# Optimization experiments

Hardware: AMD Instinct MI355X
Metric: run time of the kernel (lower is better)

## Reference

```python
import jax, jax.numpy as jnp
import numpy as np


def setup_inputs() -> dict:
    key = jax.random.key(0)
    ks = jax.random.split(key, 10)
    b, l, d, n, dc = 4, 4096, 768, 16, 4
    w = lambda k, shape, s: jax.random.normal(k, shape, jnp.float32) * s
    return {
        "x": w(ks[0], (b, l, d), 1.0),
        "state": jnp.zeros((b, d, n), jnp.float32),
        "W_in": w(ks[1], (d, 2 * d), 0.02),      # in_proj (expand_factor=2)
        "conv_w": w(ks[2], (d, dc), 0.1),          # depthwise conv1d weight [d_model, d_conv]
        "conv_b": w(ks[3], (d,), 0.02),
        "W_x": w(ks[4], (d, 2 * n), 0.02),         # x_proj -> (B, C)
        "W_dt": w(ks[5], (d, d), 0.02),
        "b_dt": w(ks[6], (d,), 0.02),
        "A_log": w(ks[7], (d, n), 0.1),
        "D": jnp.ones((d,), jnp.float32),
        "W_out": w(ks[8], (d, d), 0.02),
    }


def reference(x, state, W_in, conv_w, conv_b, W_x, W_dt, b_dt, A_log, D, W_out):
    b, l, d = x.shape
    n = A_log.shape[1]
    dc = conv_w.shape[1]

    xz = x @ W_in                              # [b,l,2d]
    x_ssm, z = jnp.split(xz, 2, axis=-1)       # each [b,l,d]

    # causal depthwise conv1d (torch pads by dc-1 both sides then truncates to l)
    xp = jnp.pad(x_ssm, ((0, 0), (dc - 1, 0), (0, 0)))
    x_conv = conv_b
    for k in range(dc):
        x_conv = x_conv + xp[:, k:k + l, :] * conv_w[:, k]
    x_ssm = jax.nn.silu(x_conv)

    A = -jnp.exp(A_log)                        # [d,n]
    dt = jax.nn.softplus(x_ssm @ W_dt + b_dt)  # [b,l,d]
    B_seq, C_seq = jnp.split(x_ssm @ W_x, 2, axis=-1)  # each [b,l,n]

    # selective scan: state[b,d,n] = state*exp(dt*A) + B*x ; y = <state,C> + D*x
    def step(s, inp):
        x_t, B_t, C_t, dt_t = inp              # [b,d],[b,n],[b,n],[b,d]
        dA = jnp.exp(dt_t[:, :, None] * A)     # [b,d,n]
        s = s * dA + B_t[:, None, :] * x_t[:, :, None]
        y = jnp.einsum('bdn,bn->bd', s, C_t) + D * x_t
        return s, y

    s0 = jnp.zeros((b, d, n), x.dtype)         # parallel_selective_scan starts from zeros
    _, ys = jax.lax.scan(
        step, s0,
        (x_ssm.transpose(1, 0, 2), B_seq.transpose(1, 0, 2),
         C_seq.transpose(1, 0, 2), dt.transpose(1, 0, 2)))
    y = ys.transpose(1, 0, 2)                  # [b,l,d]

    y = y * jax.nn.silu(z)
    out = y @ W_out
    # use_fused_ops path returns the (unchanged) incoming state as new_state
    return out, state
```

## Files before the change

kernel.cpp:

```cpp
#include <hip/hip_runtime.h>
#include <hip/hip_bf16.h>
#include <cstdint>
#include <cstddef>

constexpr int Bc = 4, Lc = 4096, Dc = 768, Nc = 16;
constexpr int M_TOT = Bc * Lc;
constexpr int NCH = 128;
constexpr int TCH = Lc / NCH;
constexpr int Kd = 768;
constexpr int TWO_D = 1536;
constexpr int NDTBC = 896;

typedef __attribute__((ext_vector_type(8))) short short8v;
typedef __attribute__((ext_vector_type(4))) float f32x4;

__device__ __forceinline__ float fexp2(float x) {
#if __has_builtin(__builtin_amdgcn_exp2f)
    return __builtin_amdgcn_exp2f(x);
#else
    return exp2f(x);
#endif
}
__device__ __forceinline__ float softplusf(float x) {
    return (x > 20.0f) ? x : __logf(1.0f + __expf(x));
}
__device__ __forceinline__ float siluf(float x) {
    return x / (1.0f + __expf(-x));
}
__device__ __forceinline__ float bf16lo(uint32_t v) {
    return __uint_as_float(v << 16);
}
__device__ __forceinline__ float bf16hi(uint32_t v) {
    return __uint_as_float(v & 0xffff0000u);
}

__device__ __forceinline__ void swizzled_tile(int& row0, int& col0)
{
    const int nwg = gridDim.x * gridDim.y;
    const int bid = blockIdx.y * gridDim.x + blockIdx.x;
    const int swz = (bid & 7) * (nwg >> 3) + (bid >> 3);
    row0 = (swz / gridDim.x) * 128;
    col0 = (swz % gridDim.x) * 128;
}

__global__ __launch_bounds__(256)
void gemm_bf16_f32(const __hip_bfloat16* __restrict__ Ab,
                   const __hip_bfloat16* __restrict__ Wt,
                   int N, float* __restrict__ out0)
{
    __shared__ __hip_bfloat16 Asm[128 * 32];
    __shared__ __hip_bfloat16 Bsm[128 * 32];
    const int tid = threadIdx.x;
    const int w = tid >> 6, lane = tid & 63;
    const int lr = lane & 15, lc = lane >> 4;
    int row0, col0;
    swizzled_tile(row0, col0);
    const int wrow = (w >> 1) * 64, wcol = (w & 1) * 64;

    const int srow = lane >> 2;
    const int scol = (lane & 3) * 8;

    f32x4 acc[4][4] = {};

    const int KT = Kd / 32;
    for (int kt = 0; kt < KT; ++kt) {
        if (kt) __syncthreads();
        #pragma unroll
        for (int i = 0; i < 2; ++i) {
            const int seg = w * 2 + i;
            const __hip_bfloat16* asrc =
                Ab + (size_t)(row0 + seg * 16 + srow) * Kd + kt * 32 + scol;
            const __hip_bfloat16* bsrc =
                Wt + (size_t)(col0 + seg * 16 + srow) * Kd + kt * 32 + scol;
            __builtin_amdgcn_global_load_lds(
                (const __attribute__((address_space(1))) void*)asrc,
                (__attribute__((address_space(3))) void*)(Asm + seg * 512), 16, 0, 0);
            __builtin_amdgcn_global_load_lds(
                (const __attribute__((address_space(1))) void*)bsrc,
                (__attribute__((address_space(3))) void*)(Bsm + seg * 512), 16, 0, 0);
        }
        asm volatile("s_waitcnt vmcnt(0)" ::: "memory");
        __syncthreads();

        short8v a[4], b[4];
        #pragma unroll
        for (int m = 0; m < 4; ++m)
            a[m] = *(const short8v*)((char*)Asm + (wrow + m * 16 + lr) * 64 + lc * 16);
        #pragma unroll
        for (int nf = 0; nf < 4; ++nf)
            b[nf] = *(const short8v*)((char*)Bsm + (wcol + nf * 16 + lr) * 64 + lc * 16);
        #pragma unroll
        for (int m = 0; m < 4; ++m)
            #pragma unroll
            for (int nf = 0; nf < 4; ++nf)
                acc[m][nf] = __builtin_amdgcn_mfma_f32_16x16x32_bf16(
                    a[m], b[nf], acc[m][nf], 0, 0, 0);
    }

    #pragma unroll
    for (int m = 0; m < 4; ++m)
        #pragma unroll
        for (int nf = 0; nf < 4; ++nf)
            #pragma unroll
            for (int j = 0; j < 4; ++j) {
                const int rg = row0 + wrow + m * 16 + lc * 4 + j;
                const int cg = col0 + wcol + nf * 16 + lr;
                out0[(size_t)rg * N + cg] = acc[m][nf][j];
            }
}

__global__ __launch_bounds__(256)
void gemm_bf16_b16(const __hip_bfloat16* __restrict__ Ab,
                   const __hip_bfloat16* __restrict__ Wt,
                   int N, __hip_bfloat16* __restrict__ outb)
{
    __shared__ __hip_bfloat16 Asm[128 * 32];
    __shared__ __hip_bfloat16 Bsm[128 * 32];
    const int tid = threadIdx.x;
    const int w = tid >> 6, lane = tid & 63;
    const int lr = lane & 15, lc = lane >> 4;
    int row0, col0;
    swizzled_tile(row0, col0);
    const int wrow = (w >> 1) * 64, wcol = (w & 1) * 64;

    const int srow = lane >> 2;
    const int scol = (lane & 3) * 8;

    f32x4 acc[4][4] = {};

    const int KT = Kd / 32;
    for (int kt = 0; kt < KT; ++kt) {
        if (kt) __syncthreads();
        #pragma unroll
        for (int i = 0; i < 2; ++i) {
            const int seg = w * 2 + i;
            const __hip_bfloat16* asrc =
                Ab + (size_t)(row0 + seg * 16 + srow) * Kd + kt * 32 + scol;
            const __hip_bfloat16* bsrc =
                Wt + (size_t)(col0 + seg * 16 + srow) * Kd + kt * 32 + scol;
            __builtin_amdgcn_global_load_lds(
                (const __attribute__((address_space(1))) void*)asrc,
                (__attribute__((address_space(3))) void*)(Asm + seg * 512), 16, 0, 0);
            __builtin_amdgcn_global_load_lds(
                (const __attribute__((address_space(1))) void*)bsrc,
                (__attribute__((address_space(3))) void*)(Bsm + seg * 512), 16, 0, 0);
        }
        asm volatile("s_waitcnt vmcnt(0)" ::: "memory");
        __syncthreads();

        short8v a[4], b[4];
        #pragma unroll
        for (int m = 0; m < 4; ++m)
            a[m] = *(const short8v*)((char*)Asm + (wrow + m * 16 + lr) * 64 + lc * 16);
        #pragma unroll
        for (int nf = 0; nf < 4; ++nf)
            b[nf] = *(const short8v*)((char*)Bsm + (wcol + nf * 16 + lr) * 64 + lc * 16);
        #pragma unroll
        for (int m = 0; m < 4; ++m)
            #pragma unroll
            for (int nf = 0; nf < 4; ++nf)
                acc[m][nf] = __builtin_amdgcn_mfma_f32_16x16x32_bf16(
                    a[m], b[nf], acc[m][nf], 0, 0, 0);
    }

    #pragma unroll
    for (int m = 0; m < 4; ++m)
        #pragma unroll
        for (int nf = 0; nf < 4; ++nf)
            #pragma unroll
            for (int j = 0; j < 4; ++j) {
                const int rg = row0 + wrow + m * 16 + lc * 4 + j;
                const int cg = col0 + wcol + nf * 16 + lr;
                outb[(size_t)rg * N + cg] = __float2bfloat16(acc[m][nf][j]);
            }
}

__global__ __launch_bounds__(256)
void to_bf16_kernel(const float* __restrict__ src, __hip_bfloat16* __restrict__ dst, int n4)
{
    const int i = blockIdx.x * 256 + threadIdx.x;
    if (i >= n4) return;
    const float4 v = ((const float4*)src)[i];
    dst[i * 4 + 0] = __float2bfloat16(v.x);
    dst[i * 4 + 1] = __float2bfloat16(v.y);
    dst[i * 4 + 2] = __float2bfloat16(v.z);
    dst[i * 4 + 3] = __float2bfloat16(v.w);
}

__global__ __launch_bounds__(256)
void wtrans_tile(const float* __restrict__ src, __hip_bfloat16* __restrict__ dst, int N)
{
    __shared__ float tile[32][33];
    const int n0 = blockIdx.x * 32, k0 = blockIdx.y * 32;
    const int tx = threadIdx.x & 31, ty = threadIdx.x >> 5;
    #pragma unroll
    for (int r = 0; r < 4; ++r) {
        const int k = ty + r * 8;
        tile[k][tx] = src[(size_t)(k0 + k) * N + n0 + tx];
    }
    __syncthreads();
    #pragma unroll
    for (int r = 0; r < 4; ++r) {
        const int n = ty + r * 8;
        dst[(size_t)(n0 + n) * Kd + k0 + tx] = __float2bfloat16(tile[tx][n]);
    }
}

__global__ __launch_bounds__(256)
void aprep_kernel(const float* __restrict__ A_log, float* __restrict__ Abuf)
{
    const int i = blockIdx.x * 256 + threadIdx.x;
    if (i < Dc * Nc) Abuf[i] = -expf(A_log[i]) * 1.4426950408889634f;
}

__global__ __launch_bounds__(256)
void conv_silu_kernel(const __hip_bfloat16* __restrict__ xz16, const float* __restrict__ cw,
                      const float* __restrict__ cb, __hip_bfloat16* __restrict__ xsb)
{
    const int ND2 = Dc / 2;
    const int idx = blockIdx.x * 256 + threadIdx.x;
    if (idx >= (M_TOT / 8) * ND2) return;
    const int d0 = (idx % ND2) * 2;
    const int r8 = idx / ND2;
    const int tb = r8 & (Lc / 8 - 1);
    const int b = r8 / (Lc / 8);
    const int t0 = tb * 8;
    const size_t rbase = (size_t)(b * Lc + t0);

    const float w00 = cw[d0 * 4 + 0], w01 = cw[d0 * 4 + 1],
                w02 = cw[d0 * 4 + 2], w03 = cw[d0 * 4 + 3];
    const float w10 = cw[d0 * 4 + 4], w11 = cw[d0 * 4 + 5],
                w12 = cw[d0 * 4 + 6], w13 = cw[d0 * 4 + 7];
    const float bias0 = cb[d0], bias1 = cb[d0 + 1];

    float a3 = 0.f, a2 = 0.f, a1 = 0.f;
    float b3 = 0.f, b2 = 0.f, b1 = 0.f;
    if (t0 >= 3) {
        const uint32_t v3 = *(const uint32_t*)(xz16 + (rbase - 3) * TWO_D + d0);
        const uint32_t v2 = *(const uint32_t*)(xz16 + (rbase - 2) * TWO_D + d0);
        const uint32_t v1 = *(const uint32_t*)(xz16 + (rbase - 1) * TWO_D + d0);
        a3 = bf16lo(v3); b3 = bf16hi(v3);
        a2 = bf16lo(v2); b2 = bf16hi(v2);
        a1 = bf16lo(v1); b1 = bf16hi(v1);
    }
    #pragma unroll
    for (int tt = 0; tt < 8; ++tt) {
        const uint32_t v0 = *(const uint32_t*)(xz16 + (rbase + tt) * TWO_D + d0);
        const float x0a = bf16lo(v0), x0b = bf16hi(v0);
        const float ra = siluf(fmaf(w03, x0a, fmaf(w02, a1, fmaf(w01, a2, fmaf(w00, a3, bias0)))));
        const float rb = siluf(fmaf(w13, x0b, fmaf(w12, b1, fmaf(w11, b2, fmaf(w10, b3, bias1)))));
        __hip_bfloat16 o2[2] = { __float2bfloat16(ra), __float2bfloat16(rb) };
        *(uint32_t*)(xsb + (rbase + tt) * Dc + d0) = *(const uint32_t*)o2;
        a3 = a2; a2 = a1; a1 = x0a;
        b3 = b2; b2 = b1; b1 = x0b;
    }
}

__global__ __launch_bounds__(256)
void scanA(float* __restrict__ dtbc, const __hip_bfloat16* __restrict__ xsb,
           const float* __restrict__ Abuf, const float* __restrict__ bdt,
           float* __restrict__ S, float* __restrict__ dcend)
{
    const int blk = blockIdx.x;
    const int dblk = blk % 3, ch = (blk / 3) % NCH, b = blk / (3 * NCH);
    const int d = dblk * 256 + threadIdx.x;
    const int t0 = ch * TCH;
    const size_t brow = (size_t)(b * Lc + t0);

    __shared__ float bcs[TCH * 32];
    {
        const int row = threadIdx.x >> 3, c4 = (threadIdx.x & 7) * 4;
        *(float4*)&bcs[row * 32 + c4] =
            *(const float4*)(dtbc + (brow + row) * NDTBC + Dc + c4);
    }
    __syncthreads();

    float A[16];
    #pragma unroll
    for (int q = 0; q < 4; ++q)
        *(float4*)&A[q * 4] = *(const float4*)(Abuf + d * 16 + q * 4);
    const float bd = bdt[d];

    float s[16];
    #pragma unroll
    for (int n = 0; n < 16; ++n) s[n] = 0.f;

    float dc = 0.f;
    #pragma unroll 4
    for (int t = 0; t < TCH; ++t) {
        const size_t doff = (brow + t) * NDTBC + d;
        const float dt = softplusf(dtbc[doff] + bd);
        dtbc[doff] = dt;
        const float x = __bfloat162float(xsb[(brow + t) * Dc + d]);
        dc += dt;
        float Bt[16];
        #pragma unroll
        for (int q = 0; q < 4; ++q)
            *(float4*)&Bt[q * 4] = *(const float4*)&bcs[t * 32 + q * 4];
        #pragma unroll
        for (int n = 0; n < 16; ++n) {
            const float dA = fexp2(dt * A[n]);
            s[n] = fmaf(s[n], dA, Bt[n] * x);
        }
    }
    const size_t g = (size_t)(b * NCH + ch) * Dc + d;
    #pragma unroll
    for (int n = 0; n < 16; ++n) S[g * 16 + n] = s[n];
    dcend[g] = dc;
}

__global__ __launch_bounds__(256)
void scanB(float* __restrict__ S_io, const float* __restrict__ dcend,
           const float* __restrict__ Abuf)
{
    const int tid = blockIdx.x * 256 + threadIdx.x;
    const int n = tid & 15;
    const int d = (tid >> 4) % Dc;
    const int b = tid / (16 * Dc);
    const float An = Abuf[d * 16 + n];
    float s = 0.f;
    for (int ch = 0; ch < NCH; ++ch) {
        const size_t g = (size_t)(b * NCH + ch) * Dc + d;
        const float sv = S_io[g * 16 + n];
        const float p  = fexp2(dcend[g] * An);
        S_io[g * 16 + n] = s;
        s = fmaf(s, p, sv);
    }
}

__global__ __launch_bounds__(256)
void scanC(const float* __restrict__ dtbc, const __hip_bfloat16* __restrict__ xsb,
           const __hip_bfloat16* __restrict__ xz16,
           const float* __restrict__ Abuf,
           const float* __restrict__ Ibuf, const float* __restrict__ Dvec,
           __hip_bfloat16* __restrict__ ybf)
{
    const int blk = blockIdx.x;
    const int dblk = blk % 3, ch = (blk / 3) % NCH, b = blk / (3 * NCH);
    const int d = dblk * 256 + threadIdx.x;
    const int t0 = ch * TCH;
    const size_t brow = (size_t)(b * Lc + t0);

    __shared__ float bcs[TCH * 32];
    {
        const int row = threadIdx.x >> 3, c4 = (threadIdx.x & 7) * 4;
        *(float4*)&bcs[row * 32 + c4] =
            *(const float4*)(dtbc + (brow + row) * NDTBC + Dc + c4);
    }
    __syncthreads();

    float A[16], s[16];
    #pragma unroll
    for (int q = 0; q < 4; ++q)
        *(float4*)&A[q * 4] = *(const float4*)(Abuf + d * 16 + q * 4);
    const size_t g = (size_t)(b * NCH + ch) * Dc + d;
    #pragma unroll
    for (int q = 0; q < 4; ++q)
        *(float4*)&s[q * 4] = *(const float4*)(Ibuf + g * 16 + q * 4);
    const float Dd = Dvec[d];

    #pragma unroll 4
    for (int t = 0; t < TCH; ++t) {
        const float dt = dtbc[(brow + t) * NDTBC + d];
        const float x  = __bfloat162float(xsb[(brow + t) * Dc + d]);
        const float z  = __bfloat162float(xz16[(brow + t) * TWO_D + Dc + d]);
        float Bt[16], Ct[16];
        #pragma unroll
        for (int q = 0; q < 4; ++q) {
            *(float4*)&Bt[q * 4] = *(const float4*)&bcs[t * 32 + q * 4];
            *(float4*)&Ct[q * 4] = *(const float4*)&bcs[t * 32 + 16 + q * 4];
        }
        float yl = fmaf(Dd, x, 0.f);
        #pragma unroll
        for (int n = 0; n < 16; ++n) {
            const float dA = fexp2(dt * A[n]);
            s[n] = fmaf(s[n], dA, Bt[n] * x);
            yl = fmaf(s[n], Ct[n], yl);
        }
        ybf[(brow + t) * Dc + d] = __float2bfloat16(yl * siluf(z));
    }
}

extern "C" void kernel_launch(void* const* d_in, const int* in_sizes, int n_in,
                              void* d_out, int out_size, void* d_ws, size_t ws_size,
                              hipStream_t stream)
{
    const float* x      = (const float*)d_in[0];
    const float* state  = (const float*)d_in[1];
    const float* W_in   = (const float*)d_in[2];
    const float* conv_w = (const float*)d_in[3];
    const float* conv_b = (const float*)d_in[4];
    const float* W_x    = (const float*)d_in[5];
    const float* W_dt   = (const float*)d_in[6];
    const float* b_dt   = (const float*)d_in[7];
    const float* A_log  = (const float*)d_in[8];
    const float* Dvec   = (const float*)d_in[9];
    const float* W_out  = (const float*)d_in[10];
    float* out = (float*)d_out;

    char* wsb = (char*)d_ws;
    __hip_bfloat16* xz16 = (__hip_bfloat16*)wsb;     wsb += (size_t)M_TOT * TWO_D * 2;
    float* dtbc  = (float*)wsb;                      wsb += (size_t)M_TOT * NDTBC * 4;
    float* Sb    = (float*)wsb;                      wsb += (size_t)Bc * NCH * Dc * Nc * 4;
    float* dcend = (float*)wsb;                      wsb += (size_t)Bc * NCH * Dc * 4;
    __hip_bfloat16* xb  = (__hip_bfloat16*)wsb;      wsb += (size_t)M_TOT * Dc * 2;
    __hip_bfloat16* xsb = (__hip_bfloat16*)wsb;      wsb += (size_t)M_TOT * Dc * 2;
    float* Abuf = (float*)wsb;                       wsb += (size_t)Dc * Nc * 4;
    __hip_bfloat16* WinT  = (__hip_bfloat16*)wsb;    wsb += (size_t)1536 * Kd * 2;
    __hip_bfloat16* WcatT = (__hip_bfloat16*)wsb;    wsb += (size_t)NDTBC * Kd * 2;
    __hip_bfloat16* WoutT = (__hip_bfloat16*)wsb;    wsb += (size_t)768 * Kd * 2;
    float* Ib = Sb;
    __hip_bfloat16* ybf = xb;

    to_bf16_kernel<<<(M_TOT * Dc / 4 + 255) / 256, 256, 0, stream>>>(x, xb, M_TOT * Dc / 4);
    wtrans_tile<<<dim3(1536 / 32, Kd / 32), 256, 0, stream>>>(W_in, WinT, 1536);
    wtrans_tile<<<dim3(768 / 32, Kd / 32), 256, 0, stream>>>(W_dt, WcatT, 768);
    wtrans_tile<<<dim3(32 / 32, Kd / 32), 256, 0, stream>>>(W_x, WcatT + (size_t)768 * Kd, 32);
    wtrans_tile<<<dim3(768 / 32, Kd / 32), 256, 0, stream>>>(W_out, WoutT, 768);
    aprep_kernel<<<(Dc * Nc + 255) / 256, 256, 0, stream>>>(A_log, Abuf);

    gemm_bf16_b16<<<dim3(TWO_D / 128, M_TOT / 128), 256, 0, stream>>>(
        xb, WinT, TWO_D, xz16);
    conv_silu_kernel<<<((M_TOT / 8) * (Dc / 2) + 255) / 256, 256, 0, stream>>>(
        xz16, conv_w, conv_b, xsb);
    gemm_bf16_f32<<<dim3(NDTBC / 128, M_TOT / 128), 256, 0, stream>>>(
        xsb, WcatT, NDTBC, dtbc);
    scanA<<<Bc * NCH * 3, 256, 0, stream>>>(dtbc, xsb, Abuf, b_dt, Sb, dcend);
    scanB<<<(Bc * Dc * Nc) / 256, 256, 0, stream>>>(Sb, dcend, Abuf);
    scanC<<<Bc * NCH * 3, 256, 0, stream>>>(dtbc, xsb, xz16, Abuf, Ib, Dvec, ybf);
    gemm_bf16_f32<<<dim3(Dc / 128, M_TOT / 128), 256, 0, stream>>>(ybf, WoutT, Dc, out);
    hipMemcpyAsync(out + (size_t)M_TOT * Dc, state,
                   (size_t)(Bc * Dc * Nc) * sizeof(float),
                   hipMemcpyDeviceToDevice, stream);
}
```

Measured before the change: 279.9 us.

## Double GEMM K-tile to 64 with XOR-swizzled LDS layout

```diff
diff --git a/kernel.cpp b/kernel.cpp
--- a/kernel.cpp
+++ b/kernel.cpp
@@ -48,8 +48,8 @@
                    const __hip_bfloat16* __restrict__ Wt,
                    int N, float* __restrict__ out0)
 {
-    __shared__ __hip_bfloat16 Asm[128 * 32];
-    __shared__ __hip_bfloat16 Bsm[128 * 32];
+    __shared__ __hip_bfloat16 Asm[128 * 64];
+    __shared__ __hip_bfloat16 Bsm[128 * 64];
     const int tid = threadIdx.x;
     const int w = tid >> 6, lane = tid & 63;
     const int lr = lane & 15, lc = lane >> 4;
@@ -57,44 +57,49 @@
     swizzled_tile(row0, col0);
     const int wrow = (w >> 1) * 64, wcol = (w & 1) * 64;
 
-    const int srow = lane >> 2;
-    const int scol = (lane & 3) * 8;
+    const int grow = lane >> 3;
+    const int gcol = 8 * ((lane & 7) ^ (lane >> 3));
+    const int rsw = (lr & 7) << 4;
 
     f32x4 acc[4][4] = {};
 
-    const int KT = Kd / 32;
+    const int KT = Kd / 64;
     for (int kt = 0; kt < KT; ++kt) {
         if (kt) __syncthreads();
         #pragma unroll
-        for (int i = 0; i < 2; ++i) {
-            const int seg = w * 2 + i;
+        for (int i = 0; i < 4; ++i) {
+            const int g = w * 4 + i;
             const __hip_bfloat16* asrc =
-                Ab + (size_t)(row0 + seg * 16 + srow) * Kd + kt * 32 + scol;
+                Ab + (size_t)(row0 + g * 8 + grow) * Kd + kt * 64 + gcol;
             const __hip_bfloat16* bsrc =
-                Wt + (size_t)(col0 + seg * 16 + srow) * Kd + kt * 32 + scol;
+                Wt + (size_t)(col0 + g * 8 + grow) * Kd + kt * 64 + gcol;
             __builtin_amdgcn_global_load_lds(
                 (const __attribute__((address_space(1))) void*)asrc,
-                (__attribute__((address_space(3))) void*)(Asm + seg * 512), 16, 0, 0);
+                (__attribute__((address_space(3))) void*)(Asm + g * 512), 16, 0, 0);
             __builtin_amdgcn_global_load_lds(
                 (const __attribute__((address_space(1))) void*)bsrc,
-                (__attribute__((address_space(3))) void*)(Bsm + seg * 512), 16, 0, 0);
+                (__attribute__((address_space(3))) void*)(Bsm + g * 512), 16, 0, 0);
         }
         asm volatile("s_waitcnt vmcnt(0)" ::: "memory");
         __syncthreads();
 
-        short8v a[4], b[4];
-        #pragma unroll
-        for (int m = 0; m < 4; ++m)
-            a[m] = *(const short8v*)((char*)Asm + (wrow + m * 16 + lr) * 64 + lc * 16);
-        #pragma unroll
-        for (int nf = 0; nf < 4; ++nf)
-            b[nf] = *(const short8v*)((char*)Bsm + (wcol + nf * 16 + lr) * 64 + lc * 16);
-        #pragma unroll
-        for (int m = 0; m < 4; ++m)
+        #pragma unroll
+        for (int kk = 0; kk < 2; ++kk) {
+            const int rq = (kk * 64 + lc * 16) ^ rsw;
+            short8v a[4], b[4];
+            #pragma unroll
+            for (int m = 0; m < 4; ++m)
+                a[m] = *(const short8v*)((char*)Asm + (wrow + m * 16 + lr) * 128 + rq);
             #pragma unroll
             for (int nf = 0; nf < 4; ++nf)
-                acc[m][nf] = __builtin_amdgcn_mfma_f32_16x16x32_bf16(
-                    a[m], b[nf], acc[m][nf], 0, 0, 0);
+                b[nf] = *(const short8v*)((char*)Bsm + (wcol + nf * 16 + lr) * 128 + rq);
+            #pragma unroll
+            for (int m = 0; m < 4; ++m)
+                #pragma unroll
+                for (int nf = 0; nf < 4; ++nf)
+                    acc[m][nf] = __builtin_amdgcn_mfma_f32_16x16x32_bf16(
+                        a[m], b[nf], acc[m][nf], 0, 0, 0);
+        }
     }
 
     #pragma unroll
@@ -114,8 +119,8 @@
                    const __hip_bfloat16* __restrict__ Wt,
                    int N, __hip_bfloat16* __restrict__ outb)
 {
-    __shared__ __hip_bfloat16 Asm[128 * 32];
-    __shared__ __hip_bfloat16 Bsm[128 * 32];
+    __shared__ __hip_bfloat16 Asm[128 * 64];
+    __shared__ __hip_bfloat16 Bsm[128 * 64];
     const int tid = threadIdx.x;
     const int w = tid >> 6, lane = tid & 63;
     const int lr = lane & 15, lc = lane >> 4;
@@ -123,44 +128,49 @@
     swizzled_tile(row0, col0);
     const int wrow = (w >> 1) * 64, wcol = (w & 1) * 64;
 
-    const int srow = lane >> 2;
-    const int scol = (lane & 3) * 8;
+    const int grow = lane >> 3;
+    const int gcol = 8 * ((lane & 7) ^ (lane >> 3));
+    const int rsw = (lr & 7) << 4;
 
     f32x4 acc[4][4] = {};
 
-    const int KT = Kd / 32;
+    const int KT = Kd / 64;
     for (int kt = 0; kt < KT; ++kt) {
         if (kt) __syncthreads();
         #pragma unroll
-        for (int i = 0; i < 2; ++i) {
-            const int seg = w * 2 + i;
+        for (int i = 0; i < 4; ++i) {
+            const int g = w * 4 + i;
             const __hip_bfloat16* asrc =
-                Ab + (size_t)(row0 + seg * 16 + srow) * Kd + kt * 32 + scol;
+                Ab + (size_t)(row0 + g * 8 + grow) * Kd + kt * 64 + gcol;
             const __hip_bfloat16* bsrc =
-                Wt + (size_t)(col0 + seg * 16 + srow) * Kd + kt * 32 + scol;
+                Wt + (size_t)(col0 + g * 8 + grow) * Kd + kt * 64 + gcol;
             __builtin_amdgcn_global_load_lds(
                 (const __attribute__((address_space(1))) void*)asrc,
-                (__attribute__((address_space(3))) void*)(Asm + seg * 512), 16, 0, 0);
+                (__attribute__((address_space(3))) void*)(Asm + g * 512), 16, 0, 0);
             __builtin_amdgcn_global_load_lds(
                 (const __attribute__((address_space(1))) void*)bsrc,
-                (__attribute__((address_space(3))) void*)(Bsm + seg * 512), 16, 0, 0);
+                (__attribute__((address_space(3))) void*)(Bsm + g * 512), 16, 0, 0);
         }
         asm volatile("s_waitcnt vmcnt(0)" ::: "memory");
         __syncthreads();
 
-        short8v a[4], b[4];
-        #pragma unroll
-        for (int m = 0; m < 4; ++m)
-            a[m] = *(const short8v*)((char*)Asm + (wrow + m * 16 + lr) * 64 + lc * 16);
-        #pragma unroll
-        for (int nf = 0; nf < 4; ++nf)
-            b[nf] = *(const short8v*)((char*)Bsm + (wcol + nf * 16 + lr) * 64 + lc * 16);
-        #pragma unroll
-        for (int m = 0; m < 4; ++m)
+        #pragma unroll
+        for (int kk = 0; kk < 2; ++kk) {
+            const int rq = (kk * 64 + lc * 16) ^ rsw;
+            short8v a[4], b[4];
+            #pragma unroll
+            for (int m = 0; m < 4; ++m)
+                a[m] = *(const short8v*)((char*)Asm + (wrow + m * 16 + lr) * 128 + rq);
             #pragma unroll
             for (int nf = 0; nf < 4; ++nf)
-                acc[m][nf] = __builtin_amdgcn_mfma_f32_16x16x32_bf16(
-                    a[m], b[nf], acc[m][nf], 0, 0, 0);
+                b[nf] = *(const short8v*)((char*)Bsm + (wcol + nf * 16 + lr) * 128 + rq);
+            #pragma unroll
+            for (int m = 0; m < 4; ++m)
+                #pragma unroll
+                for (int nf = 0; nf < 4; ++nf)
+                    acc[m][nf] = __builtin_amdgcn_mfma_f32_16x16x32_bf16(
+                        a[m], b[nf], acc[m][nf], 0, 0, 0);
+        }
     }
 
     #pragma unroll
```

New measurement: 260.5 us. 6.9% less time.
